# Kernel tuning notes

Hardware: AMD Instinct MI355X
Metric: run time of the kernel (lower is better)

The kernel has to match this reference:

```python
import jax, jax.numpy as jnp
import numpy as np

T = 4096      # document tokens
D = 768       # embedding dim
L = 10        # max span length (compute_idx_spans L=10)
H = 150       # Score FFNN hidden size
N = T * L     # number of candidate spans


def setup_inputs() -> dict:
    key = jax.random.key(0)
    ks = jax.random.split(key, 8)
    # all spans of length 1..L starting at every token, ends clipped to doc
    starts = np.repeat(np.arange(T), L)
    ends = np.minimum(starts + np.tile(np.arange(L), T), T - 1)
    s = 0.02
    return {
        "embeds": jax.random.normal(ks[0], (T, D), jnp.float32),
        "span_starts": jnp.asarray(starts, jnp.int32),
        "span_ends": jnp.asarray(ends, jnp.int32),
        "W_a1": jax.random.normal(ks[1], (D, H), jnp.float32) * s,
        "b_a1": jnp.zeros((H,), jnp.float32),
        "W_a2": jax.random.normal(ks[2], (H, 1), jnp.float32) * s,
        "b_a2": jnp.zeros((1,), jnp.float32),
        "W_m1": jax.random.normal(ks[3], (3 * D, H), jnp.float32) * s,
        "b_m1": jnp.zeros((H,), jnp.float32),
        "W_m2": jax.random.normal(ks[4], (H, 1), jnp.float32) * s,
        "b_m2": jnp.zeros((1,), jnp.float32),
    }


def _score(x, W1, b1, W2, b2):
    # Score module: Linear -> ReLU -> (Dropout, identity at eval) -> Linear
    return jax.nn.relu(x @ W1 + b1) @ W2 + b2


def reference(embeds, span_starts, span_ends, W_a1, b_a1, W_a2, b_a2,
              W_m1, b_m1, W_m2, b_m2):
    # per-token attention logits: [T]
    attns = _score(embeds, W_a1, b_a1, W_a2, b_a2)[:, 0]
    # ragged spans padded to fixed L with validity mask
    offs = jnp.arange(L, dtype=span_starts.dtype)
    idx_raw = span_starts[:, None] + offs[None, :]            # [N, L]
    valid = idx_raw <= span_ends[:, None]                      # [N, L]
    idx = jnp.minimum(idx_raw, T - 1)
    # pad_and_stack(attns, value=-1e10) + softmax over span positions
    a = jnp.where(valid, attns[idx], -1e10)                    # [N, L]
    w = jax.nn.softmax(a, axis=1)                              # [N, L]
    # pad_and_stack(embeds, value=0) then weighted sum
    e = jnp.where(valid[..., None], embeds[idx], 0.0)          # [N, L, D]
    attn_embeds = jnp.einsum('nl,nld->nd', w, e)               # [N, D]
    # start/end token embeddings concat with attention-pooled embedding
    g_i = jnp.concatenate(
        [embeds[span_starts], embeds[span_ends], attn_embeds], axis=1)  # [N, 3D]
    mention_scores = _score(g_i, W_m1, b_m1, W_m2, b_m2)       # [N, 1]
    return g_i, mention_scores
```

## Files before the change

kernel.cpp:

```cpp
#include <hip/hip_runtime.h>
#include <hip/hip_bf16.h>

#define T_TOK 4096
#define D_DIM 768
#define L_SPAN 10
#define H_HID 150
#define N_SPANS (T_TOK * L_SPAN)
#define GDIM 2304
#define WROWS 640
#define YCOLS 480

typedef __attribute__((ext_vector_type(8))) short bf16x8;
typedef __attribute__((ext_vector_type(4))) float f32x4;

using bf16_t = __hip_bfloat16;

static __device__ __forceinline__ short f2b(float x) {
  __hip_bfloat16 h = __float2bfloat16(x);
  short r;
  __builtin_memcpy(&r, &h, 2);
  return r;
}

__global__ void prep_kernel(const float* __restrict__ W_a1,
                            const float* __restrict__ W_m1,
                            bf16_t* __restrict__ Wt) {
  const int total = WROWS * D_DIM;
  for (int i = blockIdx.x * blockDim.x + threadIdx.x; i < total;
       i += gridDim.x * blockDim.x) {
    const int n = i / D_DIM;
    const int k = i - n * D_DIM;
    const int g = n / 160;
    const int cj = n - g * 160;
    float v = 0.f;
    if (cj < H_HID) {
      v = (g == 0) ? W_a1[k * H_HID + cj]
                   : W_m1[(k + (g - 1) * D_DIM) * H_HID + cj];
    }
    Wt[i] = __float2bfloat16(v);
  }
}

__global__ __launch_bounds__(256) void token_gemm_kernel(
    const float* __restrict__ E, const bf16_t* __restrict__ Wt,
    float* __restrict__ Y, float* __restrict__ attns,
    const float* __restrict__ b_a1, const float* __restrict__ W_a2,
    const float* __restrict__ b_a2) {
  const int wave = threadIdx.x >> 6;
  const int lane = threadIdx.x & 63;
  const int m16 = lane & 15;
  const int quad = lane >> 4;
  const int rowBase = blockIdx.x * 16;
  const int cs = wave * 160;

  const float* Arow = E + (long)(rowBase + m16) * D_DIM + quad * 8;
  const bf16_t* Wq = Wt + (long)(cs + m16) * D_DIM + quad * 8;

  f32x4 acc[10];
#pragma unroll
  for (int nt = 0; nt < 10; ++nt) acc[nt] = (f32x4){0.f, 0.f, 0.f, 0.f};

  for (int kk = 0; kk < D_DIM / 32; ++kk) {
    const f32x4 f0 = *(const f32x4*)(Arow + kk * 32);
    const f32x4 f1 = *(const f32x4*)(Arow + kk * 32 + 4);
    bf16x8 a;
    a[0] = f2b(f0.x); a[1] = f2b(f0.y); a[2] = f2b(f0.z); a[3] = f2b(f0.w);
    a[4] = f2b(f1.x); a[5] = f2b(f1.y); a[6] = f2b(f1.z); a[7] = f2b(f1.w);
#pragma unroll
    for (int nt = 0; nt < 10; ++nt) {
      const bf16x8 b = *(const bf16x8*)(Wq + (long)nt * 16 * D_DIM + kk * 32);
      acc[nt] = __builtin_amdgcn_mfma_f32_16x16x32_bf16(a, b, acc[nt], 0, 0, 0);
    }
  }

  if (wave == 0) {
    float s[4] = {0.f, 0.f, 0.f, 0.f};
#pragma unroll
    for (int nt = 0; nt < 10; ++nt) {
      const int c = nt * 16 + m16;
      float b1c = 0.f, w2c = 0.f;
      if (c < H_HID) { b1c = b_a1[c]; w2c = W_a2[c]; }
#pragma unroll
      for (int r = 0; r < 4; ++r) {
        const float h = acc[nt][r] + b1c;
        s[r] += (h > 0.f ? h : 0.f) * w2c;
      }
    }
#pragma unroll
    for (int m = 1; m <= 8; m <<= 1) {
#pragma unroll
      for (int r = 0; r < 4; ++r) s[r] += __shfl_xor(s[r], m, 64);
    }
    if (m16 == 0) {
      const float b2f = b_a2[0];
#pragma unroll
      for (int r = 0; r < 4; ++r)
        attns[rowBase + quad * 4 + r] = s[r] + b2f;
    }
  } else {
    const int cs2 = (wave - 1) * 160;
#pragma unroll
    for (int nt = 0; nt < 10; ++nt) {
#pragma unroll
      for (int r = 0; r < 4; ++r) {
        const int row = rowBase + quad * 4 + r;
        Y[(long)row * YCOLS + cs2 + nt * 16 + m16] = acc[nt][r];
      }
    }
  }
}

__global__ __launch_bounds__(256) void span_kernel(
    const float* __restrict__ embeds, const int* __restrict__ ends,
    const float* __restrict__ Y, const float* __restrict__ attns,
    const float* __restrict__ b_m1, const float* __restrict__ W_m2,
    const float* __restrict__ b_m2, float* __restrict__ g,
    float* __restrict__ scores) {
  __shared__ float E[L_SPAN][D_DIM];
  __shared__ float Ys[L_SPAN][YCOLS];
  __shared__ float att[L_SPAN];
  __shared__ float wts[L_SPAN][L_SPAN];
  __shared__ int sE[L_SPAN];

  const int t = blockIdx.x;
  const int tid = threadIdx.x;

  for (int idx = tid; idx < L_SPAN * 192; idx += 256) {
    const int i = idx / 192, d = idx - i * 192;
    const int r = min(t + i, T_TOK - 1);
    ((f32x4*)E)[idx] = ((const f32x4*)(embeds + (long)r * D_DIM))[d];
  }
  for (int idx = tid; idx < L_SPAN * 120; idx += 256) {
    const int i = idx / 120, d = idx - i * 120;
    const int r = min(t + i, T_TOK - 1);
    ((f32x4*)Ys)[idx] = ((const f32x4*)(Y + (long)r * YCOLS))[d];
  }
  if (tid < L_SPAN) {
    att[tid] = attns[min(t + tid, T_TOK - 1)];
    sE[tid] = ends[t * L_SPAN + tid];
  }
  __syncthreads();

  if (tid < L_SPAN) {
    const int v = sE[tid] - t + 1;
    float mx = att[0];
    for (int o = 1; o < v; ++o) mx = fmaxf(mx, att[o]);
    float den = 0.f;
    for (int o = 0; o < v; ++o) den += __expf(att[o] - mx);
    const float inv = 1.f / den;
    for (int o = 0; o < L_SPAN; ++o)
      wts[tid][o] = (o < v) ? __expf(att[o] - mx) * inv : 0.f;
  }
  __syncthreads();

  {
    const int wave = tid >> 6, lane = tid & 63;
    for (int l = wave; l < L_SPAN; l += 4) {
      const int ie = sE[l] - t;
      float p = 0.f;
      for (int c = lane; c < H_HID; c += 64) {
        float h = Ys[0][c] + Ys[ie][160 + c] + b_m1[c];
#pragma unroll
        for (int o = 0; o < L_SPAN; ++o) h += wts[l][o] * Ys[o][320 + c];
        p += (h > 0.f ? h : 0.f) * W_m2[c];
      }
#pragma unroll
      for (int m = 1; m <= 32; m <<= 1) p += __shfl_xor(p, m, 64);
      if (lane == 0) scores[t * L_SPAN + l] = p + b_m2[0];
    }
  }

  const f32x4* E4 = (const f32x4*)E;
#pragma unroll
  for (int l = 0; l < L_SPAN; ++l) {
    f32x4* g4 = (f32x4*)(g + ((long)t * L_SPAN + l) * GDIM);
    const int ie = sE[l] - t;
    float w[L_SPAN];
#pragma unroll
    for (int o = 0; o < L_SPAN; ++o) w[o] = wts[l][o];
    for (int off = tid; off < 576; off += 256) {
      f32x4 v;
      if (off < 192) {
        v = E4[off];
      } else if (off < 384) {
        v = E4[ie * 192 + off - 192];
      } else {
        const int d = off - 384;
        f32x4 a = {0.f, 0.f, 0.f, 0.f};
#pragma unroll
        for (int o = 0; o < L_SPAN; ++o) {
          const f32x4 e = E4[o * 192 + d];
          a.x += w[o] * e.x; a.y += w[o] * e.y;
          a.z += w[o] * e.z; a.w += w[o] * e.w;
        }
        v = a;
      }
      __builtin_nontemporal_store(v, g4 + off);
    }
  }
}

extern "C" void kernel_launch(void* const* d_in, const int* in_sizes, int n_in,
                              void* d_out, int out_size, void* d_ws,
                              size_t ws_size, hipStream_t stream) {
  const float* embeds = (const float*)d_in[0];
  const int* ends = (const int*)d_in[2];
  const float* W_a1 = (const float*)d_in[3];
  const float* b_a1 = (const float*)d_in[4];
  const float* W_a2 = (const float*)d_in[5];
  const float* b_a2 = (const float*)d_in[6];
  const float* W_m1 = (const float*)d_in[7];
  const float* b_m1 = (const float*)d_in[8];
  const float* W_m2 = (const float*)d_in[9];
  const float* b_m2 = (const float*)d_in[10];

  char* ws = (char*)d_ws;
  bf16_t* Wt = (bf16_t*)ws;
  float* Y = (float*)(ws + 983040);
  float* attns = (float*)(ws + 983040 + 7864320);

  float* g_out = (float*)d_out;
  float* score_out = g_out + (long)N_SPANS * GDIM;

  prep_kernel<<<480, 256, 0, stream>>>(W_a1, W_m1, Wt);
  token_gemm_kernel<<<T_TOK / 16, 256, 0, stream>>>(embeds, Wt, Y, attns,
                                                    b_a1, W_a2, b_a2);
  span_kernel<<<T_TOK, 256, 0, stream>>>(embeds, ends, Y, attns, b_m1, W_m2,
                                         b_m2, g_out, score_out);
}
```

Baseline: 501.7 us.

## Specialize span kernel waves and pre-pack weights in MFMA fragment layout

The span kernel no longer stages the ten embedding rows in shared memory. Three waves each own a column slice: they read embeds directly, accumulate the attention-pooled sums for all ten spans in registers, and stream out g. A fourth wave loads the projected Y rows and computes the mention scores, so the score work overlaps the bandwidth-bound output writes. The token GEMM now uses 8 waves per block with the A tile converted once into LDS. The weights are pre-packed into MFMA lane order so B loads are contiguous, at the cost of a cross-wave reduction of the attention logits through shared memory.

```diff
diff --git a/kernel.cpp b/kernel.cpp
--- a/kernel.cpp
+++ b/kernel.cpp
@@ -7,8 +7,9 @@
 #define H_HID 150
 #define N_SPANS (T_TOK * L_SPAN)
 #define GDIM 2304
-#define WROWS 640
 #define YCOLS 480
+#define NC16 40
+#define KK24 24
 
 typedef __attribute__((ext_vector_type(8))) short bf16x8;
 typedef __attribute__((ext_vector_type(4))) float f32x4;
@@ -24,60 +25,80 @@
 
 __global__ void prep_kernel(const float* __restrict__ W_a1,
                             const float* __restrict__ W_m1,
-                            bf16_t* __restrict__ Wt) {
-  const int total = WROWS * D_DIM;
-  for (int i = blockIdx.x * blockDim.x + threadIdx.x; i < total;
-       i += gridDim.x * blockDim.x) {
-    const int n = i / D_DIM;
-    const int k = i - n * D_DIM;
-    const int g = n / 160;
-    const int cj = n - g * 160;
-    float v = 0.f;
-    if (cj < H_HID) {
-      v = (g == 0) ? W_a1[k * H_HID + cj]
-                   : W_m1[(k + (g - 1) * D_DIM) * H_HID + cj];
-    }
-    Wt[i] = __float2bfloat16(v);
-  }
-}
-
-__global__ __launch_bounds__(256) void token_gemm_kernel(
-    const float* __restrict__ E, const bf16_t* __restrict__ Wt,
+                            bf16_t* __restrict__ Bp) {
+  const int total = NC16 * KK24 * 64;
+  for (int s = blockIdx.x * blockDim.x + threadIdx.x; s < total;
+       s += gridDim.x * blockDim.x) {
+    const int c16 = s / (KK24 * 64);
+    const int rem = s - c16 * (KK24 * 64);
+    const int kk = rem >> 6;
+    const int l = rem & 63;
+    const int j = c16 * 16 + (l & 15);
+    const int k0 = ((l >> 4) << 3) + kk * 32;
+    const int grp = j / 160;
+    const int cj = j - grp * 160;
+    bf16x8 out;
+#pragma unroll
+    for (int e = 0; e < 8; ++e) {
+      float v = 0.f;
+      if (cj < H_HID) {
+        const int k = k0 + e;
+        v = (grp == 0) ? W_a1[k * H_HID + cj]
+                       : W_m1[(k + (grp - 1) * D_DIM) * H_HID + cj];
+      }
+      out[e] = f2b(v);
+    }
+    ((bf16x8*)Bp)[s] = out;
+  }
+}
+
+__global__ __launch_bounds__(512) void token_gemm_kernel(
+    const float* __restrict__ E, const bf16_t* __restrict__ Bp,
     float* __restrict__ Y, float* __restrict__ attns,
     const float* __restrict__ b_a1, const float* __restrict__ W_a2,
     const float* __restrict__ b_a2) {
-  const int wave = threadIdx.x >> 6;
-  const int lane = threadIdx.x & 63;
+  __shared__ __align__(16) bf16_t As[16][776];
+  __shared__ float part[2][16];
+
+  const int tid = threadIdx.x;
+  const int wave = tid >> 6;
+  const int lane = tid & 63;
   const int m16 = lane & 15;
   const int quad = lane >> 4;
   const int rowBase = blockIdx.x * 16;
-  const int cs = wave * 160;
-
-  const float* Arow = E + (long)(rowBase + m16) * D_DIM + quad * 8;
-  const bf16_t* Wq = Wt + (long)(cs + m16) * D_DIM + quad * 8;
-
-  f32x4 acc[10];
-#pragma unroll
-  for (int nt = 0; nt < 10; ++nt) acc[nt] = (f32x4){0.f, 0.f, 0.f, 0.f};
-
-  for (int kk = 0; kk < D_DIM / 32; ++kk) {
-    const f32x4 f0 = *(const f32x4*)(Arow + kk * 32);
-    const f32x4 f1 = *(const f32x4*)(Arow + kk * 32 + 4);
+
+  for (int idx = tid; idx < 16 * 96; idx += 512) {
+    const int r = idx / 96;
+    const int c8 = idx - r * 96;
+    const float* src = E + (long)(rowBase + r) * D_DIM + c8 * 8;
+    const f32x4 f0 = *(const f32x4*)src;
+    const f32x4 f1 = *(const f32x4*)(src + 4);
     bf16x8 a;
     a[0] = f2b(f0.x); a[1] = f2b(f0.y); a[2] = f2b(f0.z); a[3] = f2b(f0.w);
     a[4] = f2b(f1.x); a[5] = f2b(f1.y); a[6] = f2b(f1.z); a[7] = f2b(f1.w);
-#pragma unroll
-    for (int nt = 0; nt < 10; ++nt) {
-      const bf16x8 b = *(const bf16x8*)(Wq + (long)nt * 16 * D_DIM + kk * 32);
+    *(bf16x8*)&As[r][c8 * 8] = a;
+  }
+  __syncthreads();
+
+  f32x4 acc[5];
+#pragma unroll
+  for (int nt = 0; nt < 5; ++nt) acc[nt] = (f32x4){0.f, 0.f, 0.f, 0.f};
+
+  for (int kk = 0; kk < KK24; ++kk) {
+    const bf16x8 a = *(const bf16x8*)&As[m16][quad * 8 + kk * 32];
+#pragma unroll
+    for (int nt = 0; nt < 5; ++nt) {
+      const bf16x8 b = *(const bf16x8*)(
+          Bp + ((long)((wave * 5 + nt) * KK24 + kk) * 64 + lane) * 8);
       acc[nt] = __builtin_amdgcn_mfma_f32_16x16x32_bf16(a, b, acc[nt], 0, 0, 0);
     }
   }
 
-  if (wave == 0) {
+  if (wave < 2) {
     float s[4] = {0.f, 0.f, 0.f, 0.f};
 #pragma unroll
-    for (int nt = 0; nt < 10; ++nt) {
-      const int c = nt * 16 + m16;
+    for (int nt = 0; nt < 5; ++nt) {
+      const int c = (wave * 5 + nt) * 16 + m16;
       float b1c = 0.f, w2c = 0.f;
       if (c < H_HID) { b1c = b_a1[c]; w2c = W_a2[c]; }
 #pragma unroll
@@ -92,22 +113,22 @@
       for (int r = 0; r < 4; ++r) s[r] += __shfl_xor(s[r], m, 64);
     }
     if (m16 == 0) {
-      const float b2f = b_a2[0];
-#pragma unroll
-      for (int r = 0; r < 4; ++r)
-        attns[rowBase + quad * 4 + r] = s[r] + b2f;
+#pragma unroll
+      for (int r = 0; r < 4; ++r) part[wave][quad * 4 + r] = s[r];
     }
   } else {
-    const int cs2 = (wave - 1) * 160;
-#pragma unroll
-    for (int nt = 0; nt < 10; ++nt) {
+    const int c0 = wave * 80 - 160;
+#pragma unroll
+    for (int nt = 0; nt < 5; ++nt) {
 #pragma unroll
       for (int r = 0; r < 4; ++r) {
-        const int row = rowBase + quad * 4 + r;
-        Y[(long)row * YCOLS + cs2 + nt * 16 + m16] = acc[nt][r];
-      }
-    }
-  }
+        Y[(long)(rowBase + quad * 4 + r) * YCOLS + c0 + nt * 16 + m16] =
+            acc[nt][r];
+      }
+    }
+  }
+  __syncthreads();
+  if (tid < 16) attns[rowBase + tid] = part[0][tid] + part[1][tid] + b_a2[0];
 }
 
 __global__ __launch_bounds__(256) void span_kernel(
@@ -116,86 +137,87 @@
     const float* __restrict__ b_m1, const float* __restrict__ W_m2,
     const float* __restrict__ b_m2, float* __restrict__ g,
     float* __restrict__ scores) {
-  __shared__ float E[L_SPAN][D_DIM];
-  __shared__ float Ys[L_SPAN][YCOLS];
-  __shared__ float att[L_SPAN];
-  __shared__ float wts[L_SPAN][L_SPAN];
-  __shared__ int sE[L_SPAN];
+  __shared__ __align__(16) float Ys[L_SPAN][YCOLS];
+  __shared__ __align__(16) float wtsT[L_SPAN][12];
+  __shared__ int sIE[L_SPAN];
 
   const int t = blockIdx.x;
   const int tid = threadIdx.x;
-
-  for (int idx = tid; idx < L_SPAN * 192; idx += 256) {
-    const int i = idx / 192, d = idx - i * 192;
-    const int r = min(t + i, T_TOK - 1);
-    ((f32x4*)E)[idx] = ((const f32x4*)(embeds + (long)r * D_DIM))[d];
-  }
-  for (int idx = tid; idx < L_SPAN * 120; idx += 256) {
-    const int i = idx / 120, d = idx - i * 120;
-    const int r = min(t + i, T_TOK - 1);
-    ((f32x4*)Ys)[idx] = ((const f32x4*)(Y + (long)r * YCOLS))[d];
+  const int wave = tid >> 6;
+  const int lane = tid & 63;
+
+  if (wave == 3) {
+    for (int idx = lane; idx < L_SPAN * 120; idx += 64) {
+      const int i = idx / 120, dd = idx - i * 120;
+      const int r = min(t + i, T_TOK - 1);
+      ((f32x4*)Ys)[idx] = ((const f32x4*)(Y + (long)r * YCOLS))[dd];
+    }
   }
   if (tid < L_SPAN) {
-    att[tid] = attns[min(t + tid, T_TOK - 1)];
-    sE[tid] = ends[t * L_SPAN + tid];
+    float a[L_SPAN];
+#pragma unroll
+    for (int o = 0; o < L_SPAN; ++o) a[o] = attns[min(t + o, T_TOK - 1)];
+    const int ie = ends[t * L_SPAN + tid] - t;
+    sIE[tid] = ie;
+    float mx = a[0];
+    for (int o = 1; o <= ie; ++o) mx = fmaxf(mx, a[o]);
+    float den = 0.f;
+    for (int o = 0; o <= ie; ++o) den += __expf(a[o] - mx);
+    const float inv = 1.f / den;
+#pragma unroll
+    for (int o = 0; o < L_SPAN; ++o)
+      wtsT[o][tid] = (o <= ie) ? __expf(a[o] - mx) * inv : 0.f;
   }
   __syncthreads();
 
-  if (tid < L_SPAN) {
-    const int v = sE[tid] - t + 1;
-    float mx = att[0];
-    for (int o = 1; o < v; ++o) mx = fmaxf(mx, att[o]);
-    float den = 0.f;
-    for (int o = 0; o < v; ++o) den += __expf(att[o] - mx);
-    const float inv = 1.f / den;
-    for (int o = 0; o < L_SPAN; ++o)
-      wts[tid][o] = (o < v) ? __expf(att[o] - mx) * inv : 0.f;
-  }
-  __syncthreads();
-
-  {
-    const int wave = tid >> 6, lane = tid & 63;
-    for (int l = wave; l < L_SPAN; l += 4) {
-      const int ie = sE[l] - t;
+  if (wave < 3) {
+    const int d = tid;
+    f32x4 acc[L_SPAN];
+#pragma unroll
+    for (int l = 0; l < L_SPAN; ++l) acc[l] = (f32x4){0.f, 0.f, 0.f, 0.f};
+
+#pragma unroll
+    for (int o = 0; o < L_SPAN; ++o) {
+      const int r = min(t + o, T_TOK - 1);
+      const f32x4 e = *(const f32x4*)(embeds + (long)r * D_DIM + d * 4);
+      const f32x4 w0 = *(const f32x4*)&wtsT[o][0];
+      const f32x4 w4 = *(const f32x4*)&wtsT[o][4];
+      const f32x4 w8 = *(const f32x4*)&wtsT[o][8];
+      acc[0] += e * w0.x; acc[1] += e * w0.y;
+      acc[2] += e * w0.z; acc[3] += e * w0.w;
+      acc[4] += e * w4.x; acc[5] += e * w4.y;
+      acc[6] += e * w4.z; acc[7] += e * w4.w;
+      acc[8] += e * w8.x; acc[9] += e * w8.y;
+    }
+
+    const f32x4 e0 = *(const f32x4*)(embeds + (long)t * D_DIM + d * 4);
+    float* gbase = g + (long)t * L_SPAN * GDIM + d * 4;
+#pragma unroll
+    for (int l = 0; l < L_SPAN; ++l) {
+      float* go = gbase + (long)l * GDIM;
+      const int re = t + sIE[l];
+      const f32x4 ee = *(const f32x4*)(embeds + (long)re * D_DIM + d * 4);
+      __builtin_nontemporal_store(e0, (f32x4*)go);
+      __builtin_nontemporal_store(ee, (f32x4*)(go + D_DIM));
+      __builtin_nontemporal_store(acc[l], (f32x4*)(go + 2 * D_DIM));
+    }
+  } else {
+    const float bm2 = b_m2[0];
+    for (int l = 0; l < L_SPAN; ++l) {
+      const int ie = sIE[l];
+      float wl[L_SPAN];
+#pragma unroll
+      for (int o = 0; o < L_SPAN; ++o) wl[o] = wtsT[o][l];
       float p = 0.f;
       for (int c = lane; c < H_HID; c += 64) {
         float h = Ys[0][c] + Ys[ie][160 + c] + b_m1[c];
 #pragma unroll
-        for (int o = 0; o < L_SPAN; ++o) h += wts[l][o] * Ys[o][320 + c];
+        for (int o = 0; o < L_SPAN; ++o) h += wl[o] * Ys[o][320 + c];
         p += (h > 0.f ? h : 0.f) * W_m2[c];
       }
 #pragma unroll
       for (int m = 1; m <= 32; m <<= 1) p += __shfl_xor(p, m, 64);
-      if (lane == 0) scores[t * L_SPAN + l] = p + b_m2[0];
-    }
-  }
-
-  const f32x4* E4 = (const f32x4*)E;
-#pragma unroll
-  for (int l = 0; l < L_SPAN; ++l) {
-    f32x4* g4 = (f32x4*)(g + ((long)t * L_SPAN + l) * GDIM);
-    const int ie = sE[l] - t;
-    float w[L_SPAN];
-#pragma unroll
-    for (int o = 0; o < L_SPAN; ++o) w[o] = wts[l][o];
-    for (int off = tid; off < 576; off += 256) {
-      f32x4 v;
-      if (off < 192) {
-        v = E4[off];
-      } else if (off < 384) {
-        v = E4[ie * 192 + off - 192];
-      } else {
-        const int d = off - 384;
-        f32x4 a = {0.f, 0.f, 0.f, 0.f};
-#pragma unroll
-        for (int o = 0; o < L_SPAN; ++o) {
-          const f32x4 e = E4[o * 192 + d];
-          a.x += w[o] * e.x; a.y += w[o] * e.y;
-          a.z += w[o] * e.z; a.w += w[o] * e.w;
-        }
-        v = a;
-      }
-      __builtin_nontemporal_store(v, g4 + off);
+      if (lane == 0) scores[t * L_SPAN + l] = p + bm2;
     }
   }
 }
@@ -215,15 +237,15 @@
   const float* b_m2 = (const float*)d_in[10];
 
   char* ws = (char*)d_ws;
-  bf16_t* Wt = (bf16_t*)ws;
+  bf16_t* Bp = (bf16_t*)ws;
   float* Y = (float*)(ws + 983040);
   float* attns = (float*)(ws + 983040 + 7864320);
 
   float* g_out = (float*)d_out;
   float* score_out = g_out + (long)N_SPANS * GDIM;
 
-  prep_kernel<<<480, 256, 0, stream>>>(W_a1, W_m1, Wt);
-  token_gemm_kernel<<<T_TOK / 16, 256, 0, stream>>>(embeds, Wt, Y, attns,
+  prep_kernel<<<240, 256, 0, stream>>>(W_a1, W_m1, Bp);
+  token_gemm_kernel<<<T_TOK / 16, 512, 0, stream>>>(embeds, Bp, Y, attns,
                                                     b_a1, W_a2, b_a2);
   span_kernel<<<T_TOK, 256, 0, stream>>>(embeds, ends, Y, attns, b_m1, W_m2,
                                          b_m2, g_out, score_out);
```

New measurement: 434.1 us. 13.5% less time.
